# Kernel optimization log

Hardware: AMD Instinct MI355X
Metric: run time of the kernel (lower is better)

The kernel has to match this reference:

```python
import jax, jax.numpy as jnp
import numpy as np

EMB, HID, NCH, CHK = 512, 1024, 16, 64   # hid_sz=1024, chunk_sz=64 -> 16 chunks
K, V = 5, 32000                           # n_mixtures, vocab
B, T = 8, 129
GATE = 4 * HID + 2 * NCH                  # i,f,o,g plus 2 master gates over chunks


def setup_inputs() -> dict:
    key = jax.random.key(0)
    ks = jax.random.split(key, 12)
    w = lambda k, shape: jax.random.normal(k, shape, jnp.float32) * 0.05
    return {
        "ys_token": jax.random.randint(ks[0], (B, T), 0, V),
        "emb": w(ks[1], (V, EMB)).at[0].set(0.0),  # padding_idx=0 row zeroed
        "Wx0": w(ks[2], (EMB, GATE)), "Wh0": w(ks[3], (HID, GATE)), "b0": jnp.zeros((GATE,), jnp.float32),
        "Wx1": w(ks[4], (HID, GATE)), "Wh1": w(ks[5], (HID, GATE)), "b1": jnp.zeros((GATE,), jnp.float32),
        "Wx2": w(ks[6], (HID, GATE)), "Wh2": w(ks[7], (HID, GATE)), "b2": jnp.zeros((GATE,), jnp.float32),
        "Wp": w(ks[8], (HID, K)), "bp": jnp.zeros((K,), jnp.float32),
        "Wl": w(ks[9], (HID, K * HID)), "bl": jnp.zeros((K * HID,), jnp.float32),
        "Wo": w(ks[10], (HID, V)), "bo": jnp.zeros((V,), jnp.float32),
    }


def _onlstm_cell(x, h, c, Wx, Wh, b):
    """One ON-LSTM step. Returns (h', c', master_forget_cumax)."""
    proj = x @ Wx + h @ Wh + b
    gates, masters = proj[:, : 4 * HID], proj[:, 4 * HID :]
    i, f, o, g = jnp.split(gates, 4, axis=-1)
    i, f, o = jax.nn.sigmoid(i), jax.nn.sigmoid(f), jax.nn.sigmoid(o)
    g = jnp.tanh(g)
    mf, mi = jnp.split(masters, 2, axis=-1)            # (B, NCH) each
    tf = jnp.cumsum(jax.nn.softmax(mf, -1), -1)        # master forget: cumax
    ti = 1.0 - jnp.cumsum(jax.nn.softmax(mi, -1), -1)  # master input: 1 - cumax
    tfe = jnp.repeat(tf, CHK, axis=-1)                 # expand chunks to HID
    tie = jnp.repeat(ti, CHK, axis=-1)
    w_ = tfe * tie
    c2 = (f * w_ + (tfe - w_)) * c + (i * w_ + (tie - w_)) * g
    h2 = o * jnp.tanh(c2)
    return h2, c2, tf


def reference(ys_token, emb, Wx0, Wh0, b0, Wx1, Wh1, b1, Wx2, Wh2, b2, Wp, bp, Wl, bl, Wo, bo):
    ys_in = ys_token[:, :-1]
    x = emb[ys_in]                                     # (B, T-1, EMB)
    z = jnp.zeros((B, HID), jnp.float32)

    def step(carry, xt):
        h0, c0, h1, c1, h2, c2 = carry
        h0, c0, _ = _onlstm_cell(xt, h0, c0, Wx0, Wh0, b0)
        h1, c1, tf1 = _onlstm_cell(h0, h1, c1, Wx1, Wh1, b1)  # s_layer = 1
        h2, c2, _ = _onlstm_cell(h1, h2, c2, Wx2, Wh2, b2)
        df = NCH - jnp.sum(tf1, -1)                    # expected split depth (B,)
        return (h0, c0, h1, c1, h2, c2), (h2, tf1, df)

    _, (outs, cf, df) = jax.lax.scan(step, (z, z, z, z, z, z), jnp.swapaxes(x, 0, 1))
    h = jnp.swapaxes(outs, 0, 1)                       # (B, L, HID)
    cf = jnp.swapaxes(cf, 0, 1)                        # (B, L, NCH)
    df = jnp.swapaxes(df, 0, 1)                        # (B, L)

    # Mixture-of-Softmaxes predictor
    log_prior = jax.nn.log_softmax(h @ Wp + bp, -1)    # (B, L, K)
    lat = jnp.tanh(h @ Wl + bl).reshape(B, T - 1, K, HID)
    mix = jax.nn.log_softmax(jnp.einsum("blkh,hv->blkv", lat, Wo) + bo, -1)
    logp = jax.nn.logsumexp(log_prior[..., None] + mix, axis=2)  # (B, L, V) log-probs

    gold = ys_token[:, 1:]
    mask = (gold != 0).astype(jnp.float32)
    nll = -jnp.take_along_axis(logp, gold[..., None], -1)[..., 0]
    per_seq = jnp.sum(nll * mask, 1) / (jnp.sum(mask, 1) + 1e-13)
    loss = jnp.mean(per_seq)
    pred = jnp.argmax(logp, -1)
    return loss, df, cf, pred
```

## Files before the change

### kernel.cpp

```cpp
#include <hip/hip_runtime.h>
#include <stdint.h>
#include <stddef.h>

#define TT   128
#define GATE 4128
#define VOC  32000
#define NWG  256

typedef float  f32x4 __attribute__((ext_vector_type(4)));
typedef short  bf16x8 __attribute__((ext_vector_type(8)));
typedef unsigned short u16x4 __attribute__((ext_vector_type(4)));

__device__ __forceinline__ float bf2f(ushort u){
  union { uint32_t i; float f; } c; c.i = ((uint32_t)u) << 16; return c.f;
}
__device__ __forceinline__ ushort f2bf(float x){
  uint32_t u = __builtin_bit_cast(uint32_t, x);
  uint32_t r = (u + 0x7fffu + ((u >> 16) & 1u)) >> 16;
  return (ushort)r;
}

__global__ void embed_kernel(const int* __restrict__ ys, const float* __restrict__ emb,
                             float* __restrict__ x){
  int r = blockIdx.x;
  int t = r >> 3, b = r & 7;
  int tok = ys[b*129 + t];
  f32x4 v = *(const f32x4*)&emb[(size_t)tok*512 + threadIdx.x*4];
  *(f32x4*)&x[(size_t)r*512 + threadIdx.x*4] = v;
}

__global__ void whT_kernel(const float* __restrict__ Wh, float* __restrict__ WhT){
  __shared__ float tile[32][33];
  int g0 = blockIdx.x*32, k0 = blockIdx.y*32;
  int tx = threadIdx.x, ty = threadIdx.y;
  for (int i = ty; i < 32; i += 8)
    tile[i][tx] = Wh[(size_t)(k0+i)*GATE + g0 + tx];
  __syncthreads();
  for (int i = ty; i < 32; i += 8)
    WhT[(size_t)(g0+i)*1024 + k0 + tx] = tile[tx][i];
}

__global__ void whmT_kernel(const float* __restrict__ Wh, float* __restrict__ WhmT){
  int idx = blockIdx.x*256 + threadIdx.x;
  int k = idx >> 5, c = idx & 31;
  WhmT[idx] = Wh[(size_t)k*GATE + 4096 + c];
}

__global__ __launch_bounds__(256) void wosplit_kernel(const float* __restrict__ Wo,
                                                      uint32_t* __restrict__ hi_img,
                                                      uint32_t* __restrict__ lo_img){
  __shared__ float tile[32][132];
  int ks = blockIdx.x, nt = blockIdx.y;
  int tid = threadIdx.x;
  for (int i = tid; i < 4096; i += 256)
    tile[i>>7][i&127] = Wo[(size_t)(ks*32 + (i>>7))*VOC + nt*128 + (i&127)];
  __syncthreads();
  size_t base = ((size_t)(nt*32 + ks)) << 11;
  for (int i = tid; i < 2048; i += 256){
    int p = i*4;
    int row = p >> 6, kgpos = (p >> 4) & 3, sub = (p >> 2) & 3;
    int kg = kgpos ^ ((row >> 1) & 3);
    int ke = kg*8 + 2*sub;
    float x0 = tile[ke][row], x1 = tile[ke+1][row];
    ushort h0 = f2bf(x0), h1 = f2bf(x1);
    ushort l0 = f2bf(x0 - bf2f(h0)), l1 = f2bf(x1 - bf2f(h1));
    hi_img[base + i] = (uint32_t)h0 | ((uint32_t)h1 << 16);
    lo_img[base + i] = (uint32_t)l0 | ((uint32_t)l1 << 16);
  }
}

template<int MODE>
__global__ __launch_bounds__(256) void gemm_f32_kernel(
    const float* __restrict__ X, const float* __restrict__ W, const float* __restrict__ bias,
    float* __restrict__ O1, ushort* __restrict__ O2, ushort* __restrict__ O3,
    int Kdim, int N)
{
  __shared__ float At[2][8][132];
  __shared__ float Bs[2][8][132];
  int tid = threadIdx.x;
  int n0 = blockIdx.x*128, r0 = blockIdx.y*128;
  int tx = tid & 15, ty = tid >> 4;
  int am = tid >> 1, akq = tid & 1;
  int bk = tid >> 5, bnc = tid & 31;
  float acc[8][8];
  #pragma unroll
  for (int i=0;i<8;i++)
    #pragma unroll
    for (int j=0;j<8;j++) acc[i][j]=0.f;
  {
    f32x4 av = *(const f32x4*)&X[(size_t)(r0+am)*Kdim + akq*4];
    At[0][akq*4+0][am]=av.x; At[0][akq*4+1][am]=av.y; At[0][akq*4+2][am]=av.z; At[0][akq*4+3][am]=av.w;
    int nb = n0 + bnc*4;
    f32x4 bv = {0.f,0.f,0.f,0.f};
    if (nb + 3 < N) bv = *(const f32x4*)&W[(size_t)bk*N + nb];
    *(f32x4*)&Bs[0][bk][bnc*4] = bv;
  }
  __syncthreads();
  int nk = Kdim >> 3;
  for (int ksb = 0; ksb < nk; ksb++){
    int cb = ksb & 1;
    if (ksb + 1 < nk){
      int k0 = (ksb+1)*8, bs = cb^1;
      f32x4 av = *(const f32x4*)&X[(size_t)(r0+am)*Kdim + k0 + akq*4];
      At[bs][akq*4+0][am]=av.x; At[bs][akq*4+1][am]=av.y; At[bs][akq*4+2][am]=av.z; At[bs][akq*4+3][am]=av.w;
      int nb = n0 + bnc*4;
      f32x4 bv = {0.f,0.f,0.f,0.f};
      if (nb + 3 < N) bv = *(const f32x4*)&W[(size_t)(k0+bk)*N + nb];
      *(f32x4*)&Bs[bs][bk][bnc*4] = bv;
    }
    #pragma unroll
    for (int k = 0; k < 8; k++){
      float a[8], b[8];
      *(f32x4*)&a[0] = *(const f32x4*)&At[cb][k][ty*8];
      *(f32x4*)&a[4] = *(const f32x4*)&At[cb][k][ty*8+4];
      *(f32x4*)&b[0] = *(const f32x4*)&Bs[cb][k][tx*8];
      *(f32x4*)&b[4] = *(const f32x4*)&Bs[cb][k][tx*8+4];
      #pragma unroll
      for (int i=0;i<8;i++)
        #pragma unroll
        for (int j=0;j<8;j++) acc[i][j] = fmaf(a[i], b[j], acc[i][j]);
    }
    __syncthreads();
  }
  #pragma unroll
  for (int i=0;i<8;i++){
    int r = r0 + ty*8 + i;
    #pragma unroll
    for (int j=0;j<8;j+=4){
      int n = n0 + tx*8 + j;
      if (n + 3 < N){
        f32x4 v;
        v.x = acc[i][j+0] + bias[n+0];
        v.y = acc[i][j+1] + bias[n+1];
        v.z = acc[i][j+2] + bias[n+2];
        v.w = acc[i][j+3] + bias[n+3];
        if (MODE >= 1){
          v.x = tanhf(v.x); v.y = tanhf(v.y); v.z = tanhf(v.z); v.w = tanhf(v.w);
        }
        *(f32x4*)&O1[(size_t)r*N + n] = v;
        if (MODE == 2){
          u16x4 h, l;
          #pragma unroll
          for (int q = 0; q < 4; q++){
            ushort hb = f2bf(v[q]);
            h[q] = hb;
            l[q] = f2bf(v[q] - bf2f(hb));
          }
          *(u16x4*)&O2[(size_t)r*N + n] = h;
          *(u16x4*)&O3[(size_t)r*N + n] = l;
        }
      }
    }
  }
}

__device__ __forceinline__ void gbar(int* flags, int* gen, int ep, int wg, int tid){
  if (wg == 0){
    if (tid == 0){
      __threadfence();
      __hip_atomic_store(&flags[0], ep, __ATOMIC_RELAXED, __HIP_MEMORY_SCOPE_AGENT);
    }
    if (tid < NWG){
      while (__hip_atomic_load(&flags[tid*16], __ATOMIC_RELAXED, __HIP_MEMORY_SCOPE_AGENT) < ep)
        __builtin_amdgcn_s_sleep(1);
    }
    __syncthreads();
    if (tid == 0){
      __threadfence();
      __hip_atomic_store(gen, ep, __ATOMIC_RELAXED, __HIP_MEMORY_SCOPE_AGENT);
      __threadfence();
    }
  } else {
    if (tid == 0){
      __threadfence();
      __hip_atomic_store(&flags[wg*16], ep, __ATOMIC_RELAXED, __HIP_MEMORY_SCOPE_AGENT);
      while (__hip_atomic_load(gen, __ATOMIC_RELAXED, __HIP_MEMORY_SCOPE_AGENT) < ep)
        __builtin_amdgcn_s_sleep(2);
      __threadfence();
    }
  }
}

__global__ __launch_bounds__(512) void scan_kernel(
    const float* __restrict__ A,
    const float* __restrict__ WhT,
    const float* __restrict__ WhmT,
    float* __restrict__ hbuf,
    float* __restrict__ H,
    float* __restrict__ cf_out, float* __restrict__ df_out,
    int* bar_flags, int* bar_gen, int* mflags, float* tfti)
{
  __shared__ __align__(16) float wls[1024*20];
  __shared__ __align__(16) float hls[1024*12];
  __shared__ __align__(16) float gpw[2][2][32][36];
  __shared__ float projg[8][16];
  __shared__ float cst[8][4];
  __shared__ float mpart[8][8][4];
  __shared__ float projmb[32];

  int tid = threadIdx.x, wg = blockIdx.x;
  int e0 = wg*4, chunk = wg >> 4;

  #pragma unroll
  for (int c = 0; c < 16; c++){
    int gcol = (c>>2)*1024 + e0 + (c&3);
    const float* src = WhT + (size_t)gcol*1024;
    for (int k = tid; k < 1024; k += 512)
      wls[k*20 + c] = src[k];
  }
  if (tid < 32) cst[tid & 7][tid >> 3] = 0.f;
  __syncthreads();

  int cq = tid >> 8;
  int bh = (tid >> 7) & 1;
  int kp = tid & 127;
  bool isM = (wg < 8);
  int mcg = tid & 7, mkp = tid >> 3;

  for (int t = 0; t < TT; t++){
    int rb = (t+1) & 1, wb = t & 1;
    float Ag = 0.f;
    if (tid < 128){
      int c = tid >> 3, b = tid & 7;
      Ag = A[(size_t)(t*8+b)*GATE + (c>>2)*1024 + e0 + (c&3)];
    }
    float Am = 0.f;
    if (isM && tid < 32) Am = A[(size_t)(t*8+wg)*GATE + 4096 + tid];

    {
      const f32x4* hb4 = (const f32x4*)&hbuf[rb*8192];
      #pragma unroll
      for (int s2 = 0; s2 < 4; s2++){
        int i4 = s2*512 + tid;
        f32x4 v = hb4[i4];
        int k = i4 >> 1, h2 = i4 & 1;
        *(f32x4*)&hls[k*12 + h2*4] = v;
      }
    }
    __syncthreads();

    if (isM){
      float macc[4] = {0.f,0.f,0.f,0.f};
      #pragma unroll
      for (int j = 0; j < 16; j++){
        int k = j*64 + mkp;
        f32x4 wm = *(const f32x4*)&WhmT[k*32 + mcg*4];
        float hv = hls[k*12 + wg];
        macc[0] += wm.x*hv; macc[1] += wm.y*hv; macc[2] += wm.z*hv; macc[3] += wm.w*hv;
      }
      #pragma unroll
      for (int off = 8; off < 64; off <<= 1){
        macc[0] += __shfl_xor(macc[0], off);
        macc[1] += __shfl_xor(macc[1], off);
        macc[2] += __shfl_xor(macc[2], off);
        macc[3] += __shfl_xor(macc[3], off);
      }
      if ((tid & 63) < 8){
        int wv = tid >> 6;
        mpart[wv][mcg][0] = macc[0]; mpart[wv][mcg][1] = macc[1];
        mpart[wv][mcg][2] = macc[2]; mpart[wv][mcg][3] = macc[3];
      }
      __syncthreads();
      if (tid < 32){
        float s = Am;
        #pragma unroll
        for (int wv = 0; wv < 8; wv++) s += mpart[wv][tid>>2][tid&3];
        projmb[tid] = s;
      }
      __syncthreads();
      if (tid < 32){
        int half = tid >> 4, j = tid & 15;
        float x = projmb[tid];
        float mx = x;
        #pragma unroll
        for (int o = 1; o < 16; o <<= 1) mx = fmaxf(mx, __shfl_xor(mx, o));
        float e = expf(x - mx);
        float ssum = e;
        #pragma unroll
        for (int o = 1; o < 16; o <<= 1) ssum += __shfl_xor(ssum, o);
        float sm = e / ssum;
        float c = sm;
        #pragma unroll
        for (int o = 1; o < 16; o <<= 1){
          float t2 = __shfl_up(c, o);
          if (j >= o) c += t2;
        }
        float outv = half ? (1.f - c) : c;
        tfti[half*128 + wg*16 + j] = outv;
        if (cf_out != nullptr && half == 0){
          cf_out[(wg*TT + t)*16 + j] = c;
          float ts = c;
          #pragma unroll
          for (int o = 1; o < 16; o <<= 1) ts += __shfl_xor(ts, o);
          if (j == 0) df_out[wg*TT + t] = 16.f - ts;
        }
      }
      __syncthreads();
      if (tid == 0){
        __threadfence();
        __hip_atomic_store(&mflags[wg*16], t+1, __ATOMIC_RELAXED, __HIP_MEMORY_SCOPE_AGENT);
      }
    }

    float acc[8][4];
    #pragma unroll
    for (int c = 0; c < 8; c++)
      #pragma unroll
      for (int b2 = 0; b2 < 4; b2++) acc[c][b2] = 0.f;
    #pragma unroll
    for (int j = 0; j < 8; j++){
      int k = j*128 + kp;
      float wa[8], hb[4];
      *(f32x4*)&wa[0] = *(const f32x4*)&wls[k*20 + cq*8];
      *(f32x4*)&wa[4] = *(const f32x4*)&wls[k*20 + cq*8 + 4];
      *(f32x4*)&hb[0] = *(const f32x4*)&hls[k*12 + bh*4];
      #pragma unroll
      for (int c = 0; c < 8; c++)
        #pragma unroll
        for (int b2 = 0; b2 < 4; b2++)
          acc[c][b2] = fmaf(wa[c], hb[b2], acc[c][b2]);
    }
    #pragma unroll
    for (int c = 0; c < 8; c++)
      #pragma unroll
      for (int b2 = 0; b2 < 4; b2++){
        float v = acc[c][b2];
        v += __shfl_xor(v, 1);
        v += __shfl_xor(v, 2);
        acc[c][b2] = v;
      }
    if ((kp & 3) == 0){
      int kg = kp >> 2;
      #pragma unroll
      for (int c = 0; c < 8; c++){
        f32x4 v4 = { acc[c][0], acc[c][1], acc[c][2], acc[c][3] };
        *(f32x4*)&gpw[cq][bh][kg][c*4] = v4;
      }
    }
    __syncthreads();
    if (tid < 128){
      int c = tid >> 3, b = tid & 7;
      float s = Ag;
      #pragma unroll
      for (int g = 0; g < 32; g++) s += gpw[c>>3][b>>2][g][(c&7)*4 + (b&3)];
      projg[b][c] = s;
    }
    if (tid < 8){
      while (__hip_atomic_load(&mflags[tid*16], __ATOMIC_RELAXED, __HIP_MEMORY_SCOPE_AGENT) < t+1)
        __builtin_amdgcn_s_sleep(1);
    }
    __syncthreads();
    if (tid < 32){
      int b = tid & 7, e = tid >> 3;
      float gi = projg[b][e], gf = projg[b][4+e], go = projg[b][8+e], gg = projg[b][12+e];
      float iv = 1.f/(1.f+expf(-gi)), fv = 1.f/(1.f+expf(-gf)), ov = 1.f/(1.f+expf(-go));
      float gv = tanhf(gg);
      float tf = __hip_atomic_load(&tfti[b*16 + chunk],       __ATOMIC_RELAXED, __HIP_MEMORY_SCOPE_AGENT);
      float ti = __hip_atomic_load(&tfti[128 + b*16 + chunk], __ATOMIC_RELAXED, __HIP_MEMORY_SCOPE_AGENT);
      float w  = tf*ti;
      float c2 = (fv*w + (tf - w))*cst[b][e] + (iv*w + (ti - w))*gv;
      cst[b][e] = c2;
      float h2 = ov * tanhf(c2);
      hbuf[wb*8192 + (e0+e)*8 + b] = h2;
      H[(size_t)(t*8+b)*1024 + e0 + e] = h2;
    }
    __syncthreads();
    gbar(bar_flags, bar_gen, t+1, wg, tid);
    __syncthreads();
  }
}

__device__ __forceinline__ void stageA_lds(const ushort* gsrc, char* ldsbase, int row0, int k0, int tid){
  int lane = tid & 63, wv = tid >> 6;
  #pragma unroll
  for (int s = 0; s < 2; s++){
    int p = wv*1024 + s*4096 + lane*16;
    int row = p >> 6;
    int kg  = (p >> 4) & 3;
    int kgs = kg ^ ((row >> 1) & 3);
    const ushort* ga = gsrc + (size_t)(row0 + row)*1024 + k0 + kgs*8;
    __builtin_amdgcn_global_load_lds(
        (const __attribute__((address_space(1))) void*)ga,
        (__attribute__((address_space(3))) void*)(ldsbase + wv*1024 + s*4096),
        16, 0, 0);
  }
}
__device__ __forceinline__ void stageB_pre(const char* img, char* lds, int nt, int ks, int tid){
  int lane = tid & 63, wv = tid >> 6;
  const char* base = img + (((size_t)(nt*32 + ks)) << 13);
  #pragma unroll
  for (int s = 0; s < 2; s++){
    int p = wv*1024 + s*4096 + lane*16;
    __builtin_amdgcn_global_load_lds(
        (const __attribute__((address_space(1))) void*)(base + p),
        (__attribute__((address_space(3))) void*)(lds + p),
        16, 0, 0);
  }
}
__device__ __forceinline__ void stageB_cv(const float* __restrict__ Wo, int n0, int k0, int tid,
                                          char* bhi, char* blo){
  int kp = tid & 15, g = tid >> 4;
  const float* src = Wo + (size_t)(k0 + 2*kp)*VOC + n0 + g*8;
  f32x4 v00 = *(const f32x4*)(src);
  f32x4 v01 = *(const f32x4*)(src + 4);
  f32x4 v10 = *(const f32x4*)(src + VOC);
  f32x4 v11 = *(const f32x4*)(src + VOC + 4);
  int kg = kp >> 2, sub = kp & 3;
  #pragma unroll
  for (int j = 0; j < 8; j++){
    float x0 = (j < 4) ? v00[j] : v01[j-4];
    float x1 = (j < 4) ? v10[j] : v11[j-4];
    ushort h0 = f2bf(x0), h1 = f2bf(x1);
    ushort l0 = f2bf(x0 - bf2f(h0)), l1 = f2bf(x1 - bf2f(h1));
    int n = g*8 + j;
    int byte = n*64 + ((kg ^ ((n >> 1) & 3)) << 4) + sub*4;
    *(uint32_t*)(bhi + byte) = (uint32_t)h0 | ((uint32_t)h1 << 16);
    *(uint32_t*)(blo + byte) = (uint32_t)l0 | ((uint32_t)l1 << 16);
  }
}
__device__ __forceinline__ bf16x8 rdfrag(const char* base, int row, int kg){
  int byte = row*64 + ((kg ^ ((row >> 1) & 3)) << 4);
  return *(const bf16x8*)(base + byte);
}

template<int PRE>
__global__ __launch_bounds__(256) void wo_gemm_kernel(
    const ushort* __restrict__ Ahi, const ushort* __restrict__ Alo,
    const float* __restrict__ Wo, const float* __restrict__ bo,
    const char* __restrict__ wohi_img, const char* __restrict__ wolo_img,
    float* __restrict__ S, float* __restrict__ partials, int rowbase)
{
  __shared__ __align__(16) char smem[66560];
  __shared__ float bo_s[128];
  __shared__ float redm[128][2], reds[128][2];
  int tid = threadIdx.x;
  int nt = blockIdx.x, mt = blockIdx.y;
  int n0 = nt*128, row0loc = mt*128, row0 = rowbase + row0loc;
  if (tid < 128) bo_s[tid] = bo[n0 + tid];
  f32x4 acc[4][4] = {};

  stageA_lds(Ahi, smem + 0,    row0, 0, tid);
  stageA_lds(Alo, smem + 8192, row0, 0, tid);
  if (PRE){
    stageB_pre(wohi_img, smem + 16384, nt, 0, tid);
    stageB_pre(wolo_img, smem + 24576, nt, 0, tid);
  } else {
    stageB_cv(Wo, n0, 0, tid, smem + 16384, smem + 24576);
  }
  __syncthreads();

  int lane = tid & 63, wv = tid >> 6;
  int wr = wv >> 1, wc = wv & 1;
  int rl = lane & 15, kgl = lane >> 4;
  for (int ks = 0; ks < 32; ks++){
    char* cb = smem + (ks & 1)*32768;
    if (ks + 1 < 32){
      char* nb2 = smem + ((ks+1) & 1)*32768;
      stageA_lds(Ahi, nb2,        row0, (ks+1)*32, tid);
      stageA_lds(Alo, nb2 + 8192, row0, (ks+1)*32, tid);
      if (PRE){
        stageB_pre(wohi_img, nb2 + 16384, nt, ks+1, tid);
        stageB_pre(wolo_img, nb2 + 24576, nt, ks+1, tid);
      } else {
        stageB_cv(Wo, n0, (ks+1)*32, tid, nb2 + 16384, nb2 + 24576);
      }
    }
    bf16x8 ah[4], al[4], bh[4], bl2[4];
    #pragma unroll
    for (int m = 0; m < 4; m++){
      int row = wr*64 + m*16 + rl;
      ah[m] = rdfrag(cb,        row, kgl);
      al[m] = rdfrag(cb + 8192, row, kgl);
    }
    #pragma unroll
    for (int n = 0; n < 4; n++){
      int rw = wc*64 + n*16 + rl;
      bh[n]  = rdfrag(cb + 16384, rw, kgl);
      bl2[n] = rdfrag(cb + 24576, rw, kgl);
    }
    #pragma unroll
    for (int m = 0; m < 4; m++)
      #pragma unroll
      for (int n = 0; n < 4; n++){
        acc[m][n] = __builtin_amdgcn_mfma_f32_16x16x32_bf16(ah[m], bh[n],  acc[m][n], 0,0,0);
        acc[m][n] = __builtin_amdgcn_mfma_f32_16x16x32_bf16(ah[m], bl2[n], acc[m][n], 0,0,0);
        acc[m][n] = __builtin_amdgcn_mfma_f32_16x16x32_bf16(al[m], bh[n],  acc[m][n], 0,0,0);
      }
    __syncthreads();
  }

  float* st = (float*)smem;
  #pragma unroll
  for (int m = 0; m < 4; m++){
    int rb = wr*64 + m*16 + (lane >> 4)*4;
    #pragma unroll
    for (int n = 0; n < 4; n++){
      int col = wc*64 + n*16 + rl;
      #pragma unroll
      for (int j = 0; j < 4; j++)
        st[(rb + j)*130 + col] = acc[m][n][j];
    }
  }
  __syncthreads();
  int row = tid >> 1, half = tid & 1;
  float lmax = -1e30f;
  for (int jc = 0; jc < 64; jc += 4){
    f32x4 v;
    #pragma unroll
    for (int j = 0; j < 4; j++){
      float x = st[row*130 + half*64 + jc + j] + bo_s[half*64 + jc + j];
      st[row*130 + half*64 + jc + j] = x;
      v[j] = x;
      lmax = fmaxf(lmax, x);
    }
    *(f32x4*)&S[(size_t)(row0loc + row)*VOC + n0 + half*64 + jc] = v;
  }
  redm[row][half] = lmax;
  __syncthreads();
  float rm = fmaxf(redm[row][0], redm[row][1]);
  float lsum = 0.f;
  for (int jc = 0; jc < 64; jc++)
    lsum += expf(st[row*130 + half*64 + jc] - rm);
  reds[row][half] = lsum;
  __syncthreads();
  if (half == 0){
    float2 pr; pr.x = rm; pr.y = reds[row][0] + reds[row][1];
    *(float2*)&partials[((size_t)(row0loc + row)*250 + nt)*2] = pr;
  }
}

__global__ void zfin_kernel(const float* __restrict__ partials, double* __restrict__ Zc, int CH){
  int rl = blockIdx.x*256 + threadIdx.x;
  if (rl >= CH) return;
  float m = -1e30f;
  for (int t2 = 0; t2 < 250; t2++) m = fmaxf(m, partials[((size_t)rl*250 + t2)*2]);
  double s = 0.0;
  for (int t2 = 0; t2 < 250; t2++){
    float pm = partials[((size_t)rl*250 + t2)*2];
    float se = partials[((size_t)rl*250 + t2)*2 + 1];
    s += exp((double)pm - (double)m)*(double)se;
  }
  Zc[rl] = (double)m + log(s);
}

__device__ __forceinline__ float cand_q(const float* __restrict__ srow, int v,
                                        float l0, float l1, float l2, float l3, float l4){
  float t0 = l0 + srow[v];
  float t1 = l1 + srow[VOC   + v];
  float t2 = l2 + srow[2*VOC + v];
  float t3 = l3 + srow[3*VOC + v];
  float t4 = l4 + srow[4*VOC + v];
  float m = fmaxf(fmaxf(fmaxf(t0,t1),fmaxf(t2,t3)),t4);
  return m + logf(expf(t0-m)+expf(t1-m)+expf(t2-m)+expf(t3-m)+expf(t4-m));
}
__global__ __launch_bounds__(256) void cand_kernel(
    const float* __restrict__ S, const double* __restrict__ lp, const double* __restrict__ Z,
    int* __restrict__ cand, int rbase)
{
  int g = blockIdx.x; int r = rbase + g; int tid = threadIdx.x;
  __shared__ float lpk[5];
  __shared__ float rq[256]; __shared__ int rv[256];
  __shared__ int cnt; __shared__ int list[64];
  if (tid < 5) lpk[tid] = (float)(lp[r*5 + tid] - Z[r*5 + tid]);
  if (tid == 0) cnt = 0;
  __syncthreads();
  float l0 = lpk[0], l1 = lpk[1], l2 = lpk[2], l3 = lpk[3], l4 = lpk[4];
  const float* srow = S + (size_t)(g*5)*VOC;
  float bq = -1e30f; int bv = 0;
  for (int v = tid; v < VOC; v += 256){
    float q = cand_q(srow, v, l0,l1,l2,l3,l4);
    if (q > bq){ bq = q; bv = v; }
  }
  rq[tid] = bq; rv[tid] = bv; __syncthreads();
  for (int s = 128; s > 0; s >>= 1){
    if (tid < s){
      if (rq[tid+s] > rq[tid] || (rq[tid+s] == rq[tid] && rv[tid+s] < rv[tid])){
        rq[tid] = rq[tid+s]; rv[tid] = rv[tid+s];
      }
    }
    __syncthreads();
  }
  float M = rq[0]; int argv = rv[0];
  for (int v = tid; v < VOC; v += 256){
    float q = cand_q(srow, v, l0,l1,l2,l3,l4);
    if (q >= M - 0.02f && v != argv){
      int ix = atomicAdd(&cnt, 1);
      if (ix < 63) list[ix] = v;
    }
  }
  __syncthreads();
  int nc = cnt < 63 ? cnt : 63;
  if (tid == 0){ cand[r*66] = nc + 1; cand[r*66 + 1] = argv; }
  if (tid < nc) cand[r*66 + 2 + tid] = list[tid];
}

__global__ __launch_bounds__(256) void refine_kernel(
    const float* __restrict__ lat, const float* __restrict__ Wo, const float* __restrict__ bo,
    const double* __restrict__ lp, const double* __restrict__ Z,
    const int* __restrict__ cand, const int* __restrict__ ys,
    float* __restrict__ nll, float* __restrict__ pred_out)
{
  int r = blockIdx.x, tid = threadIdx.x;
  int b = r & 7, l = r >> 3;
  int nc = cand[r*66];
  if (nc < 0) nc = 0;
  if (nc > 64) nc = 64;
  __shared__ double dred[5][4];
  __shared__ double bestval; __shared__ int bestv;
  if (tid == 0){ bestval = -1e300; bestv = 0; }
  __syncthreads();
  int gold = ys[b*129 + l + 1];
  for (int ci = 0; ci <= nc; ci++){
    int v = (ci < nc) ? cand[r*66 + 1 + ci] : gold;
    double p0=0,p1=0,p2=0,p3=0,p4=0;
    for (int h = tid; h < 1024; h += 256){
      double w = (double)Wo[(size_t)h*VOC + v];
      p0 += (double)lat[((size_t)r*5+0)*1024 + h]*w;
      p1 += (double)lat[((size_t)r*5+1)*1024 + h]*w;
      p2 += (double)lat[((size_t)r*5+2)*1024 + h]*w;
      p3 += (double)lat[((size_t)r*5+3)*1024 + h]*w;
      p4 += (double)lat[((size_t)r*5+4)*1024 + h]*w;
    }
    #pragma unroll
    for (int off = 32; off; off >>= 1){
      p0 += __shfl_down(p0, off); p1 += __shfl_down(p1, off);
      p2 += __shfl_down(p2, off); p3 += __shfl_down(p3, off);
      p4 += __shfl_down(p4, off);
    }
    if ((tid & 63) == 0){
      int w = tid >> 6;
      dred[0][w]=p0; dred[1][w]=p1; dred[2][w]=p2; dred[3][w]=p3; dred[4][w]=p4;
    }
    __syncthreads();
    if (tid == 0){
      double bv = (double)bo[v];
      double tk[5]; double mx = -1e300;
      #pragma unroll
      for (int k = 0; k < 5; k++){
        double sk = dred[k][0]+dred[k][1]+dred[k][2]+dred[k][3] + bv;
        tk[k] = (lp[r*5+k] - Z[r*5+k]) + sk;
        mx = tk[k] > mx ? tk[k] : mx;
      }
      double q = mx + log(exp(tk[0]-mx)+exp(tk[1]-mx)+exp(tk[2]-mx)+exp(tk[3]-mx)+exp(tk[4]-mx));
      if (ci < nc){
        if (q > bestval || (q == bestval && v < bestv)){ bestval = q; bestv = v; }
      } else {
        nll[r] = (float)(-q);
      }
    }
    __syncthreads();
  }
  if (tid == 0) pred_out[b*TT + l] = (float)bestv;
}

__global__ __launch_bounds__(64) void prior_kernel(
    const float* __restrict__ H2, const float* __restrict__ Wp, const float* __restrict__ bp,
    double* __restrict__ lp)
{
  int r = blockIdx.x, tid = threadIdx.x;
  double p0=0,p1=0,p2=0,p3=0,p4=0;
  for (int h = tid; h < 1024; h += 64){
    double x = (double)H2[(size_t)r*1024 + h];
    const float* w = &Wp[h*5];
    p0 += x*(double)w[0]; p1 += x*(double)w[1]; p2 += x*(double)w[2];
    p3 += x*(double)w[3]; p4 += x*(double)w[4];
  }
  #pragma unroll
  for (int off = 32; off; off >>= 1){
    p0 += __shfl_down(p0, off); p1 += __shfl_down(p1, off);
    p2 += __shfl_down(p2, off); p3 += __shfl_down(p3, off);
    p4 += __shfl_down(p4, off);
  }
  if (tid == 0){
    double lg[5] = { p0+(double)bp[0], p1+(double)bp[1], p2+(double)bp[2], p3+(double)bp[3], p4+(double)bp[4] };
    double mx = lg[0];
    #pragma unroll
    for (int k = 1; k < 5; k++) mx = lg[k] > mx ? lg[k] : mx;
    double s = 0;
    #pragma unroll
    for (int k = 0; k < 5; k++) s += exp(lg[k]-mx);
    double lse = mx + log(s);
    #pragma unroll
    for (int k = 0; k < 5; k++) lp[r*5+k] = lg[k] - lse;
  }
}

__global__ void loss_kernel(const float* __restrict__ nll, const int* __restrict__ ys,
                            float* __restrict__ out){
  int tid = threadIdx.x;
  __shared__ float ps[8];
  if (tid < 8){
    float s = 0.f, ms = 0.f;
    for (int l = 0; l < TT; l++){
      int gold = ys[tid*129 + l + 1];
      float m = (gold != 0) ? 1.f : 0.f;
      s  += nll[l*8 + tid]*m;
      ms += m;
    }
    ps[tid] = s/(ms + 1e-13f);
  }
  __syncthreads();
  if (tid == 0){
    float t = 0.f;
    for (int b = 0; b < 8; b++) t += ps[b];
    out[0] = t/8.f;
  }
}

extern "C" void kernel_launch(void* const* d_in, const int* in_sizes, int n_in,
                              void* d_out, int out_size, void* d_ws, size_t ws_size,
                              hipStream_t stream)
{
  (void)in_sizes; (void)n_in; (void)out_size;
  const int*   ys  = (const int*)  d_in[0];
  const float* emb = (const float*)d_in[1];
  const float* Wx0 = (const float*)d_in[2];
  const float* Wh0 = (const float*)d_in[3];
  const float* b0  = (const float*)d_in[4];
  const float* Wx1 = (const float*)d_in[5];
  const float* Wh1 = (const float*)d_in[6];
  const float* b1  = (const float*)d_in[7];
  const float* Wx2 = (const float*)d_in[8];
  const float* Wh2 = (const float*)d_in[9];
  const float* b2  = (const float*)d_in[10];
  const float* Wp  = (const float*)d_in[11];
  const float* bp  = (const float*)d_in[12];
  const float* Wl  = (const float*)d_in[13];
  const float* bl  = (const float*)d_in[14];
  const float* Wo  = (const float*)d_in[15];
  const float* bo  = (const float*)d_in[16];
  float* out = (float*)d_out;

  char* ws = (char*)d_ws;
  size_t off = 0;
  auto alloc = [&](size_t bytes){ size_t o = off; off += (bytes + 255) & ~(size_t)255; return o; };
  size_t o_hbuf = alloc(2*8192*4);
  size_t o_bars = alloc(3*(NWG*16 + 16)*sizeof(int));
  size_t o_mfl  = alloc(3*8*16*sizeof(int));
  size_t zero_bytes = off;
  size_t o_tfti = alloc(256*4);
  size_t o_x    = alloc((size_t)1024*512*4);
  size_t o_whT  = alloc((size_t)GATE*1024*4);
  size_t o_whmT = alloc((size_t)1024*32*4);
  size_t o_A    = alloc((size_t)1024*GATE*4);
  size_t o_H0   = alloc((size_t)1024*1024*4);
  size_t o_H1   = alloc((size_t)1024*1024*4);
  size_t o_H2   = alloc((size_t)1024*1024*4);
  size_t o_lp   = alloc((size_t)1024*5*8);
  size_t o_latf = alloc((size_t)1024*5120*4);
  size_t o_lath = alloc((size_t)5120*1024*2);
  size_t o_latl = alloc((size_t)5120*1024*2);
  size_t o_Z    = alloc((size_t)5120*8);
  size_t o_cand = alloc((size_t)1024*66*4);
  size_t o_nll  = alloc((size_t)1024*4);
  size_t base   = off;

  const size_t woimg = (size_t)250*32*8192;
  auto need = [&](int ch, int pre){
    return base + (pre ? 2*((woimg + 255) & ~(size_t)255) : 0)
                + (((size_t)ch*250*2*4 + 255) & ~(size_t)255)
                + (((size_t)ch*VOC*4 + 255) & ~(size_t)255);
  };
  int PRE, CH;
  if      (need(1280,1) <= ws_size){ PRE=1; CH=1280; }
  else if (need(640, 1) <= ws_size){ PRE=1; CH=640;  }
  else if (need(1280,0) <= ws_size){ PRE=0; CH=1280; }
  else                              { PRE=0; CH=640;  }
  size_t o_wohi = 0, o_wolo = 0;
  if (PRE){ o_wohi = alloc(woimg); o_wolo = alloc(woimg); }
  size_t o_part = alloc((size_t)CH*250*2*4);
  size_t o_s    = alloc((size_t)CH*VOC*4);
  (void)o_s;

  float*  hbuf  = (float*) (ws + o_hbuf);
  int*    bars  = (int*)   (ws + o_bars);
  int*    mfl   = (int*)   (ws + o_mfl);
  float*  tfti  = (float*) (ws + o_tfti);
  float*  xbuf  = (float*) (ws + o_x);
  float*  whT   = (float*) (ws + o_whT);
  float*  whmT  = (float*) (ws + o_whmT);
  float*  Abuf  = (float*) (ws + o_A);
  float*  H0    = (float*) (ws + o_H0);
  float*  H1    = (float*) (ws + o_H1);
  float*  H2    = (float*) (ws + o_H2);
  double* lpbuf = (double*)(ws + o_lp);
  float*  latf  = (float*) (ws + o_latf);
  ushort* lath  = (ushort*)(ws + o_lath);
  ushort* latl  = (ushort*)(ws + o_latl);
  double* Zbuf  = (double*)(ws + o_Z);
  int*    candb = (int*)   (ws + o_cand);
  float*  nllb  = (float*) (ws + o_nll);
  char*   wohi  = ws + o_wohi;
  char*   wolo  = ws + o_wolo;
  float*  partb = (float*) (ws + o_part);
  float*  Sbuf  = (float*) (ws + o_s);

  int perl = NWG*16 + 16;
  int* flags0 = bars;             int* gen0 = flags0 + NWG*16;
  int* flags1 = bars + perl;      int* gen1 = flags1 + NWG*16;
  int* flags2 = bars + 2*perl;    int* gen2 = flags2 + NWG*16;
  int* mfl0 = mfl;  int* mfl1 = mfl + 8*16;  int* mfl2 = mfl + 16*16;

  hipMemsetAsync(d_ws, 0, zero_bytes, stream);
  embed_kernel<<<1024, 128, 0, stream>>>(ys, emb, xbuf);
  if (PRE)
    wosplit_kernel<<<dim3(32,250), 256, 0, stream>>>(Wo, (uint32_t*)wohi, (uint32_t*)wolo);

  gemm_f32_kernel<0><<<dim3(33,8), 256, 0, stream>>>(xbuf, Wx0, b0, Abuf, nullptr, nullptr, 512, GATE);
  whT_kernel<<<dim3(129,32), dim3(32,8), 0, stream>>>(Wh0, whT);
  whmT_kernel<<<128, 256, 0, stream>>>(Wh0, whmT);
  scan_kernel<<<NWG, 512, 0, stream>>>(Abuf, whT, whmT, hbuf, H0, nullptr, nullptr,
                                       flags0, gen0, mfl0, tfti);
  gemm_f32_kernel<0><<<dim3(33,8), 256, 0, stream>>>(H0, Wx1, b1, Abuf, nullptr, nullptr, 1024, GATE);
  whT_kernel<<<dim3(129,32), dim3(32,8), 0, stream>>>(Wh1, whT);
  whmT_kernel<<<128, 256, 0, stream>>>(Wh1, whmT);
  hipMemsetAsync(hbuf, 0, 2*8192*4, stream);
  scan_kernel<<<NWG, 512, 0, stream>>>(Abuf, whT, whmT, hbuf, H1, out + 1025, out + 1,
                                       flags1, gen1, mfl1, tfti);
  gemm_f32_kernel<0><<<dim3(33,8), 256, 0, stream>>>(H1, Wx2, b2, Abuf, nullptr, nullptr, 1024, GATE);
  whT_kernel<<<dim3(129,32), dim3(32,8), 0, stream>>>(Wh2, whT);
  whmT_kernel<<<128, 256, 0, stream>>>(Wh2, whmT);
  hipMemsetAsync(hbuf, 0, 2*8192*4, stream);
  scan_kernel<<<NWG, 512, 0, stream>>>(Abuf, whT, whmT, hbuf, H2, nullptr, nullptr,
                                       flags2, gen2, mfl2, tfti);

  prior_kernel<<<1024, 64, 0, stream>>>(H2, Wp, bp, lpbuf);
  gemm_f32_kernel<2><<<dim3(40,8), 256, 0, stream>>>(H2, Wl, bl, latf, lath, latl, 1024, 5120);

  int nchunks = 5120 / CH;
  for (int c = 0; c < nchunks; c++){
    if (PRE)
      wo_gemm_kernel<1><<<dim3(250, CH/128), 256, 0, stream>>>(lath, latl, Wo, bo, wohi, wolo, Sbuf, partb, c*CH);
    else
      wo_gemm_kernel<0><<<dim3(250, CH/128), 256, 0, stream>>>(lath, latl, Wo, bo, nullptr, nullptr, Sbuf, partb, c*CH);
    zfin_kernel<<<(CH + 255)/256, 256, 0, stream>>>(partb, Zbuf + c*CH, CH);
    cand_kernel<<<CH/5, 256, 0, stream>>>(Sbuf, lpbuf, Zbuf, candb, c*(CH/5));
  }
  refine_kernel<<<1024, 256, 0, stream>>>(latf, Wo, bo, lpbuf, Zbuf, candb, ys, nllb, out + 17409);
  loss_kernel<<<1, 64, 0, stream>>>(nllb, ys, out);
}
```

Before: 9.598 ms.

## Compute master gates redundantly per workgroup and use flat all-to-all grid barrier

Every workgroup now computes the master-gate projection, softmax and cumsum for all 8 batch rows itself, instead of 8 designated workgroups computing them and publishing through global memory with a separate flag wait. The two-level gather/broadcast grid barrier is replaced by a flat barrier in which every workgroup polls all 256 flags. The next step's input projections are also prefetched before the barrier. The aim is to shorten the serial per-step critical path of the recurrence. In exchange, each workgroup does more redundant compute and reads more of WhmT, and the all-to-all flag polling puts more load on the memory system.

Measured after the change: 12.64 ms. +31.7%, slower.

```diff
diff --git a/kernel.cpp b/kernel.cpp
--- a/kernel.cpp
+++ b/kernel.cpp
@@ -154,33 +154,6 @@
   }
 }
 
-__device__ __forceinline__ void gbar(int* flags, int* gen, int ep, int wg, int tid){
-  if (wg == 0){
-    if (tid == 0){
-      __threadfence();
-      __hip_atomic_store(&flags[0], ep, __ATOMIC_RELAXED, __HIP_MEMORY_SCOPE_AGENT);
-    }
-    if (tid < NWG){
-      while (__hip_atomic_load(&flags[tid*16], __ATOMIC_RELAXED, __HIP_MEMORY_SCOPE_AGENT) < ep)
-        __builtin_amdgcn_s_sleep(1);
-    }
-    __syncthreads();
-    if (tid == 0){
-      __threadfence();
-      __hip_atomic_store(gen, ep, __ATOMIC_RELAXED, __HIP_MEMORY_SCOPE_AGENT);
-      __threadfence();
-    }
-  } else {
-    if (tid == 0){
-      __threadfence();
-      __hip_atomic_store(&flags[wg*16], ep, __ATOMIC_RELAXED, __HIP_MEMORY_SCOPE_AGENT);
-      while (__hip_atomic_load(gen, __ATOMIC_RELAXED, __HIP_MEMORY_SCOPE_AGENT) < ep)
-        __builtin_amdgcn_s_sleep(2);
-      __threadfence();
-    }
-  }
-}
-
 __global__ __launch_bounds__(512) void scan_kernel(
     const float* __restrict__ A,
     const float* __restrict__ WhT,
@@ -188,15 +161,14 @@
     float* __restrict__ hbuf,
     float* __restrict__ H,
     float* __restrict__ cf_out, float* __restrict__ df_out,
-    int* bar_flags, int* bar_gen, int* mflags, float* tfti)
+    int* bar_flags)
 {
   __shared__ __align__(16) float wls[1024*20];
   __shared__ __align__(16) float hls[1024*12];
   __shared__ __align__(16) float gpw[2][2][32][36];
   __shared__ float projg[8][16];
   __shared__ float cst[8][4];
-  __shared__ float mpart[8][8][4];
-  __shared__ float projmb[32];
+  __shared__ float tfv[8][16], tiv[8][16];
 
   int tid = threadIdx.x, wg = blockIdx.x;
   int e0 = wg*4, chunk = wg >> 4;
@@ -209,24 +181,28 @@
       wls[k*20 + c] = src[k];
   }
   if (tid < 32) cst[tid & 7][tid >> 3] = 0.f;
-  __syncthreads();
 
   int cq = tid >> 8;
   int bh = (tid >> 7) & 1;
   int kp = tid & 127;
-  bool isM = (wg < 8);
-  int mcg = tid & 7, mkp = tid >> 3;
+  int mb  = tid & 7;
+  int mcg = (tid >> 3) & 7;
+  int mks = tid >> 6;
+  float (*mscr)[8][8][4] = (float (*)[8][8][4])gpw;
+
+  float Ag = 0.f, Am = 0.f;
+  if (tid < 128){
+    int c = tid >> 3, b = tid & 7;
+    Ag = A[(size_t)b*GATE + (c>>2)*1024 + e0 + (c&3)];
+  }
+  if (tid < 256){
+    int b = tid >> 5, c = tid & 31;
+    Am = A[(size_t)b*GATE + 4096 + c];
+  }
+  __syncthreads();
 
   for (int t = 0; t < TT; t++){
     int rb = (t+1) & 1, wb = t & 1;
-    float Ag = 0.f;
-    if (tid < 128){
-      int c = tid >> 3, b = tid & 7;
-      Ag = A[(size_t)(t*8+b)*GATE + (c>>2)*1024 + e0 + (c&3)];
-    }
-    float Am = 0.f;
-    if (isM && tid < 32) Am = A[(size_t)(t*8+wg)*GATE + 4096 + tid];
-
     {
       const f32x4* hb4 = (const f32x4*)&hbuf[rb*8192];
       #pragma unroll
@@ -239,68 +215,52 @@
     }
     __syncthreads();
 
-    if (isM){
-      float macc[4] = {0.f,0.f,0.f,0.f};
-      #pragma unroll
-      for (int j = 0; j < 16; j++){
-        int k = j*64 + mkp;
+    {
+      float macc0=0.f, macc1=0.f, macc2=0.f, macc3=0.f;
+      int kb = mks*128;
+      #pragma unroll 4
+      for (int k = kb; k < kb + 128; k++){
         f32x4 wm = *(const f32x4*)&WhmT[k*32 + mcg*4];
-        float hv = hls[k*12 + wg];
-        macc[0] += wm.x*hv; macc[1] += wm.y*hv; macc[2] += wm.z*hv; macc[3] += wm.w*hv;
-      }
-      #pragma unroll
-      for (int off = 8; off < 64; off <<= 1){
-        macc[0] += __shfl_xor(macc[0], off);
-        macc[1] += __shfl_xor(macc[1], off);
-        macc[2] += __shfl_xor(macc[2], off);
-        macc[3] += __shfl_xor(macc[3], off);
-      }
-      if ((tid & 63) < 8){
-        int wv = tid >> 6;
-        mpart[wv][mcg][0] = macc[0]; mpart[wv][mcg][1] = macc[1];
-        mpart[wv][mcg][2] = macc[2]; mpart[wv][mcg][3] = macc[3];
-      }
-      __syncthreads();
-      if (tid < 32){
-        float s = Am;
+        float hv = hls[k*12 + mb];
+        macc0 = fmaf(wm.x, hv, macc0);
+        macc1 = fmaf(wm.y, hv, macc1);
+        macc2 = fmaf(wm.z, hv, macc2);
+        macc3 = fmaf(wm.w, hv, macc3);
+      }
+      f32x4 v4 = { macc0, macc1, macc2, macc3 };
+      *(f32x4*)&mscr[mb][mcg][mks][0] = v4;
+    }
+    __syncthreads();
+    if (tid < 256){
+      int b = tid >> 5, c = tid & 31;
+      float s = Am;
+      #pragma unroll
+      for (int ks = 0; ks < 8; ks++) s += mscr[b][c>>2][ks][c&3];
+      int half = (c >> 4), j = c & 15;
+      float mx = s;
+      #pragma unroll
+      for (int o = 1; o < 16; o <<= 1) mx = fmaxf(mx, __shfl_xor(mx, o));
+      float e = expf(s - mx);
+      float ssum = e;
+      #pragma unroll
+      for (int o = 1; o < 16; o <<= 1) ssum += __shfl_xor(ssum, o);
+      float sm = e / ssum;
+      float cum = sm;
+      #pragma unroll
+      for (int o = 1; o < 16; o <<= 1){
+        float t2 = __shfl_up(cum, o);
+        if (j >= o) cum += t2;
+      }
+      if (half == 0) tfv[b][j] = cum; else tiv[b][j] = 1.f - cum;
+      if (cf_out != nullptr && wg == 0 && half == 0){
+        cf_out[(b*TT + t)*16 + j] = cum;
+        float ts = cum;
         #pragma unroll
-        for (int wv = 0; wv < 8; wv++) s += mpart[wv][tid>>2][tid&3];
-        projmb[tid] = s;
-      }
-      __syncthreads();
-      if (tid < 32){
-        int half = tid >> 4, j = tid & 15;
-        float x = projmb[tid];
-        float mx = x;
-        #pragma unroll
-        for (int o = 1; o < 16; o <<= 1) mx = fmaxf(mx, __shfl_xor(mx, o));
-        float e = expf(x - mx);
-        float ssum = e;
-        #pragma unroll
-        for (int o = 1; o < 16; o <<= 1) ssum += __shfl_xor(ssum, o);
-        float sm = e / ssum;
-        float c = sm;
-        #pragma unroll
-        for (int o = 1; o < 16; o <<= 1){
-          float t2 = __shfl_up(c, o);
-          if (j >= o) c += t2;
-        }
-        float outv = half ? (1.f - c) : c;
-        tfti[half*128 + wg*16 + j] = outv;
-        if (cf_out != nullptr && half == 0){
-          cf_out[(wg*TT + t)*16 + j] = c;
-          float ts = c;
-          #pragma unroll
-          for (int o = 1; o < 16; o <<= 1) ts += __shfl_xor(ts, o);
-          if (j == 0) df_out[wg*TT + t] = 16.f - ts;
-        }
-      }
-      __syncthreads();
-      if (tid == 0){
-        __threadfence();
-        __hip_atomic_store(&mflags[wg*16], t+1, __ATOMIC_RELAXED, __HIP_MEMORY_SCOPE_AGENT);
-      }
-    }
+        for (int o = 1; o < 16; o <<= 1) ts += __shfl_xor(ts, o);
+        if (j == 0) df_out[b*TT + t] = 16.f - ts;
+      }
+    }
+    __syncthreads();
 
     float acc[8][4];
     #pragma unroll
@@ -345,18 +305,13 @@
       for (int g = 0; g < 32; g++) s += gpw[c>>3][b>>2][g][(c&7)*4 + (b&3)];
       projg[b][c] = s;
     }
-    if (tid < 8){
-      while (__hip_atomic_load(&mflags[tid*16], __ATOMIC_RELAXED, __HIP_MEMORY_SCOPE_AGENT) < t+1)
-        __builtin_amdgcn_s_sleep(1);
-    }
     __syncthreads();
     if (tid < 32){
       int b = tid & 7, e = tid >> 3;
       float gi = projg[b][e], gf = projg[b][4+e], go = projg[b][8+e], gg = projg[b][12+e];
       float iv = 1.f/(1.f+expf(-gi)), fv = 1.f/(1.f+expf(-gf)), ov = 1.f/(1.f+expf(-go));
       float gv = tanhf(gg);
-      float tf = __hip_atomic_load(&tfti[b*16 + chunk],       __ATOMIC_RELAXED, __HIP_MEMORY_SCOPE_AGENT);
-      float ti = __hip_atomic_load(&tfti[128 + b*16 + chunk], __ATOMIC_RELAXED, __HIP_MEMORY_SCOPE_AGENT);
+      float tf = tfv[b][chunk], ti = tiv[b][chunk];
       float w  = tf*ti;
       float c2 = (fv*w + (tf - w))*cst[b][e] + (iv*w + (ti - w))*gv;
       cst[b][e] = c2;
@@ -364,8 +319,27 @@
       hbuf[wb*8192 + (e0+e)*8 + b] = h2;
       H[(size_t)(t*8+b)*1024 + e0 + e] = h2;
     }
-    __syncthreads();
-    gbar(bar_flags, bar_gen, t+1, wg, tid);
+    if (t + 1 < TT){
+      if (tid < 128){
+        int c = tid >> 3, b = tid & 7;
+        Ag = A[(size_t)((t+1)*8+b)*GATE + (c>>2)*1024 + e0 + (c&3)];
+      }
+      if (tid < 256){
+        int b = tid >> 5, c = tid & 31;
+        Am = A[(size_t)((t+1)*8+b)*GATE + 4096 + c];
+      }
+    }
+    __syncthreads();
+    if (tid == 0){
+      __threadfence();
+      __hip_atomic_store(&bar_flags[wg*16], t+1, __ATOMIC_RELAXED, __HIP_MEMORY_SCOPE_AGENT);
+    }
+    if (tid < NWG){
+      while (__hip_atomic_load(&bar_flags[tid*16], __ATOMIC_RELAXED, __HIP_MEMORY_SCOPE_AGENT) < t+1)
+        __builtin_amdgcn_s_sleep(1);
+    }
+    __syncthreads();
+    if (tid == 0) __threadfence();
     __syncthreads();
   }
 }
@@ -735,10 +709,8 @@
   size_t off = 0;
   auto alloc = [&](size_t bytes){ size_t o = off; off += (bytes + 255) & ~(size_t)255; return o; };
   size_t o_hbuf = alloc(2*8192*4);
-  size_t o_bars = alloc(3*(NWG*16 + 16)*sizeof(int));
-  size_t o_mfl  = alloc(3*8*16*sizeof(int));
+  size_t o_bars = alloc(3*NWG*16*sizeof(int));
   size_t zero_bytes = off;
-  size_t o_tfti = alloc(256*4);
   size_t o_x    = alloc((size_t)1024*512*4);
   size_t o_whT  = alloc((size_t)GATE*1024*4);
   size_t o_whmT = alloc((size_t)1024*32*4);
@@ -774,8 +746,6 @@
 
   float*  hbuf  = (float*) (ws + o_hbuf);
   int*    bars  = (int*)   (ws + o_bars);
-  int*    mfl   = (int*)   (ws + o_mfl);
-  float*  tfti  = (float*) (ws + o_tfti);
   float*  xbuf  = (float*) (ws + o_x);
   float*  whT   = (float*) (ws + o_whT);
   float*  whmT  = (float*) (ws + o_whmT);
@@ -795,11 +765,9 @@
   float*  partb = (float*) (ws + o_part);
   float*  Sbuf  = (float*) (ws + o_s);
 
-  int perl = NWG*16 + 16;
-  int* flags0 = bars;             int* gen0 = flags0 + NWG*16;
-  int* flags1 = bars + perl;      int* gen1 = flags1 + NWG*16;
-  int* flags2 = bars + 2*perl;    int* gen2 = flags2 + NWG*16;
-  int* mfl0 = mfl;  int* mfl1 = mfl + 8*16;  int* mfl2 = mfl + 16*16;
+  int* flags0 = bars;
+  int* flags1 = bars + NWG*16;
+  int* flags2 = bars + 2*NWG*16;
 
   hipMemsetAsync(d_ws, 0, zero_bytes, stream);
   embed_kernel<<<1024, 128, 0, stream>>>(ys, emb, xbuf);
@@ -809,20 +777,17 @@
   gemm_f32_kernel<0><<<dim3(33,8), 256, 0, stream>>>(xbuf, Wx0, b0, Abuf, nullptr, nullptr, 512, GATE);
   whT_kernel<<<dim3(129,32), dim3(32,8), 0, stream>>>(Wh0, whT);
   whmT_kernel<<<128, 256, 0, stream>>>(Wh0, whmT);
-  scan_kernel<<<NWG, 512, 0, stream>>>(Abuf, whT, whmT, hbuf, H0, nullptr, nullptr,
-                                       flags0, gen0, mfl0, tfti);
+  scan_kernel<<<NWG, 512, 0, stream>>>(Abuf, whT, whmT, hbuf, H0, nullptr, nullptr, flags0);
   gemm_f32_kernel<0><<<dim3(33,8), 256, 0, stream>>>(H0, Wx1, b1, Abuf, nullptr, nullptr, 1024, GATE);
   whT_kernel<<<dim3(129,32), dim3(32,8), 0, stream>>>(Wh1, whT);
   whmT_kernel<<<128, 256, 0, stream>>>(Wh1, whmT);
   hipMemsetAsync(hbuf, 0, 2*8192*4, stream);
-  scan_kernel<<<NWG, 512, 0, stream>>>(Abuf, whT, whmT, hbuf, H1, out + 1025, out + 1,
-                                       flags1, gen1, mfl1, tfti);
+  scan_kernel<<<NWG, 512, 0, stream>>>(Abuf, whT, whmT, hbuf, H1, out + 1025, out + 1, flags1);
   gemm_f32_kernel<0><<<dim3(33,8), 256, 0, stream>>>(H1, Wx2, b2, Abuf, nullptr, nullptr, 1024, GATE);
   whT_kernel<<<dim3(129,32), dim3(32,8), 0, stream>>>(Wh2, whT);
   whmT_kernel<<<128, 256, 0, stream>>>(Wh2, whmT);
   hipMemsetAsync(hbuf, 0, 2*8192*4, stream);
-  scan_kernel<<<NWG, 512, 0, stream>>>(Abuf, whT, whmT, hbuf, H2, nullptr, nullptr,
-                                       flags2, gen2, mfl2, tfti);
+  scan_kernel<<<NWG, 512, 0, stream>>>(Abuf, whT, whmT, hbuf, H2, nullptr, nullptr, flags2);
 
   prior_kernel<<<1024, 64, 0, stream>>>(H2, Wp, bp, lpbuf);
   gemm_f32_kernel<2><<<dim3(40,8), 256, 0, stream>>>(H2, Wl, bl, latf, lath, latl, 1024, 5120);
```
